# Optimization experiments

Measured on AMD Instinct MI355X. Metric: run time of the kernel, lower is better.

The kernel has to match this reference:

```python
import jax, jax.numpy as jnp
import numpy as np

B, S, HID = 2, 2048, 4096
H, KV, D = 32, 8, 128          # heads, kv heads, head_dim
G = H // KV                    # num_key_value_groups
THETA = 10000.0
SCALE = 1.0 / np.sqrt(D)
NEG_INF = -1e9


def rotate_half(x):
    x1, x2 = x[..., : D // 2], x[..., D // 2 :]
    return jnp.concatenate([-x2, x1], axis=-1)


def rope_tables(seq_len):
    inv_freq = 1.0 / (THETA ** (jnp.arange(0, D, 2, dtype=jnp.float32) / D))
    t = jnp.arange(seq_len, dtype=jnp.float32)
    freqs = jnp.outer(t, inv_freq)              # [S, D/2]
    emb = jnp.concatenate([freqs, freqs], -1)   # [S, D]
    return jnp.cos(emb), jnp.sin(emb)


def setup_inputs() -> dict:
    key = jax.random.key(0)
    ks = jax.random.split(key, 5)
    w = 0.02
    x = jax.random.normal(ks[0], (B, S, HID), jnp.float32)
    Wq = jax.random.normal(ks[1], (HID, H * D), jnp.float32) * w
    Wk = jax.random.normal(ks[2], (HID, KV * D), jnp.float32) * w
    Wv = jax.random.normal(ks[3], (HID, KV * D), jnp.float32) * w
    Wo = jax.random.normal(ks[4], (H * D, HID), jnp.float32) * w
    position_ids = jnp.broadcast_to(jnp.arange(S, dtype=jnp.int32), (B, S))
    causal = jnp.where(
        jnp.arange(S)[:, None] >= jnp.arange(S)[None, :], 0.0, NEG_INF
    ).astype(jnp.float32)
    attention_mask = jnp.broadcast_to(causal, (B, 1, S, S))
    return {
        "by_pass_hidden_states": x,
        "attention_mask": attention_mask,
        "position_ids": position_ids,
        "Wq": Wq,
        "Wk": Wk,
        "Wv": Wv,
        "Wo": Wo,
    }


def reference(by_pass_hidden_states, attention_mask, position_ids, Wq, Wk, Wv, Wo):
    x = by_pass_hidden_states
    # QKV projections (weights stored [in, out])
    q = (x @ Wq).reshape(B, S, H, D).transpose(0, 2, 1, 3)    # [B,H,S,D]
    k = (x @ Wk).reshape(B, S, KV, D).transpose(0, 2, 1, 3)   # [B,KV,S,D]
    v = (x @ Wv).reshape(B, S, KV, D).transpose(0, 2, 1, 3)   # [B,KV,S,D]
    # RoPE
    cos_t, sin_t = rope_tables(S)
    cos = cos_t[position_ids][:, None]   # [B,1,S,D]
    sin = sin_t[position_ids][:, None]
    q = q * cos + rotate_half(q) * sin
    k = k * cos + rotate_half(k) * sin
    # GQA attention without materializing repeated K/V: group query heads
    qg = q.reshape(B, KV, G, S, D)
    scores = jnp.einsum("bkgsd,bktd->bkgst", qg, k) * SCALE   # [B,KV,G,S,S]
    scores = scores.reshape(B, H, S, S) + attention_mask
    probs = jax.nn.softmax(scores.astype(jnp.float32), axis=-1).astype(x.dtype)
    ctx = jnp.einsum("bkgst,bktd->bkgsd", probs.reshape(B, KV, G, S, S), v)
    ctx = ctx.reshape(B, H, S, D).transpose(0, 2, 1, 3).reshape(B, S, H * D)
    return ctx @ Wo
```

## Files before the change

### kernel.cpp

```cpp
#include <hip/hip_runtime.h>
#include <cstdint>
#include <cstddef>

#define B_   2
#define S_   2048
#define HID_ 4096
#define H_   32
#define KV_  8
#define D_   128
#define M_   (B_*S_)
#define QSTR 6144

typedef __attribute__((ext_vector_type(8))) short bf16x8;
typedef __attribute__((ext_vector_type(4))) float f32x4;
typedef __attribute__((ext_vector_type(16))) float f32x16;
typedef __attribute__((ext_vector_type(4))) unsigned int u32x4;
typedef unsigned short u16;
typedef unsigned int   u32;

#define KSC (0.08838834764831845f * 1.4426950408889634f)

__device__ __forceinline__ float bf2f(u16 v){ u32 u = ((u32)v) << 16; return __builtin_bit_cast(float, u); }
__device__ __forceinline__ u16 f2bf(float f){
  u32 u = __builtin_bit_cast(u32, f);
  u32 r = u + 0x7fffu + ((u >> 16) & 1u);
  return (u16)(r >> 16);
}

__device__ __forceinline__ void gload_lds16(const void* g, void* lds){
  __builtin_amdgcn_global_load_lds(
      (const __attribute__((address_space(1))) void*)g,
      (__attribute__((address_space(3))) void*)lds, 16, 0, 0);
}

__global__ void cast_f32_bf16(const float* __restrict__ in, u16* __restrict__ out, int n){
  int i = (blockIdx.x * blockDim.x + threadIdx.x) * 4;
  if (i >= n) return;
  float4 v = *(const float4*)(in + i);
  ushort4 o;
  o.x = f2bf(v.x); o.y = f2bf(v.y); o.z = f2bf(v.z); o.w = f2bf(v.w);
  *(ushort4*)(out + i) = o;
}

__global__ __launch_bounds__(256) void tcast(const float* __restrict__ W, u16* __restrict__ WT,
                                             int Kd, int Nd){
  __shared__ __align__(16) u16 t[64][65];
  int k0 = blockIdx.x * 64, n0 = blockIdx.y * 64;
  int lx = threadIdx.x & 15, ly = threadIdx.x >> 4;
  #pragma unroll
  for (int rr = 0; rr < 4; ++rr){
    int r = rr * 16 + ly;
    float4 v = *(const float4*)(W + (size_t)(k0 + r) * Nd + n0 + lx * 4);
    t[lx*4+0][r] = f2bf(v.x);
    t[lx*4+1][r] = f2bf(v.y);
    t[lx*4+2][r] = f2bf(v.z);
    t[lx*4+3][r] = f2bf(v.w);
  }
  __syncthreads();
  #pragma unroll
  for (int rr = 0; rr < 4; ++rr){
    int r = rr * 16 + ly;
    ushort4 o;
    o.x = t[r][lx*4+0]; o.y = t[r][lx*4+1]; o.z = t[r][lx*4+2]; o.w = t[r][lx*4+3];
    *(ushort4*)(WT + (size_t)(n0 + r) * Kd + k0 + lx * 4) = o;
  }
}

__global__ __launch_bounds__(256) void vtrans(const u16* __restrict__ QKV, u16* __restrict__ Vt){
  __shared__ __align__(16) u16 t[64][65];
  int stile = blockIdx.x;
  int b = blockIdx.y >> 4, vt = blockIdx.y & 15;
  int s0 = stile * 64, c0 = vt * 64;
  int lx = threadIdx.x & 15, ly = threadIdx.x >> 4;
  #pragma unroll
  for (int rr = 0; rr < 4; ++rr){
    int r = rr * 16 + ly;
    ushort4 v = *(const ushort4*)(QKV + (size_t)(b*S_ + s0 + r) * QSTR + 5120 + c0 + lx*4);
    t[lx*4+0][r]=v.x; t[lx*4+1][r]=v.y; t[lx*4+2][r]=v.z; t[lx*4+3][r]=v.w;
  }
  __syncthreads();
  #pragma unroll
  for (int rr = 0; rr < 4; ++rr){
    int r = rr * 16 + ly;
    ushort4 o;
    o.x=t[r][lx*4+0]; o.y=t[r][lx*4+1]; o.z=t[r][lx*4+2]; o.w=t[r][lx*4+3];
    *(ushort4*)(Vt + (size_t)(b*1024 + c0 + r) * S_ + s0 + lx*4) = o;
  }
}

__global__ void rope_k(u16* __restrict__ X, const int* __restrict__ pos, int hshift, int stride){
  int idx = blockIdx.x * 256 + threadIdx.x;
  int i = idx & 63;
  int h = (idx >> 6) & ((1 << hshift) - 1);
  int t = idx >> (6 + hshift);
  u16* p0 = X + (size_t)t * stride + h * D_ + i;
  float x1 = bf2f(p0[0]), x2 = bf2f(p0[64]);
  float fpos = (float)pos[t];
  float invf = exp2f(-(float)(2 * i) * (13.287712379549449f / 128.0f));
  float f = fpos * invf;
  float sv = __sinf(f), cv = __cosf(f);
  p0[0]  = f2bf(x1 * cv - x2 * sv);
  p0[64] = f2bf(x2 * cv + x1 * sv);
}

#define BAR() __builtin_amdgcn_s_barrier()

#define STG_A(PB, HALF, KT) do{ \
  gload_lds16(Ag + off0 + (size_t)(HALF)*1048576 + (size_t)(KT)*128, \
              (char*)smem + (PB)*32768 + (HALF)*16384 + w*1024); \
  gload_lds16(Ag + off0 + 524288 + (size_t)(HALF)*1048576 + (size_t)(KT)*128, \
              (char*)smem + (PB)*32768 + (HALF)*16384 + 8192 + w*1024); }while(0)
#define STG_B(PB, HALF, KT) do{ \
  gload_lds16(Bg + off0 + (size_t)(HALF)*1048576 + (size_t)(KT)*128, \
              (char*)smem + 65536 + (PB)*32768 + (HALF)*16384 + w*1024); \
  gload_lds16(Bg + off0 + 524288 + (size_t)(HALF)*1048576 + (size_t)(KT)*128, \
              (char*)smem + 65536 + (PB)*32768 + (HALF)*16384 + 8192 + w*1024); }while(0)

#define RD_A(DST, PP, HALF) do{ \
  _Pragma("unroll") for (int ks = 0; ks < 2; ++ks) \
  _Pragma("unroll") for (int m = 0; m < 4; ++m) \
    DST[ks][m] = *(const bf16x8*)&smem[(PP)*16384 + (HALF)*8192 + aRowBase + m*1024 + csw[ks]]; }while(0)
#define RD_B(DST, PP, HALF) do{ \
  _Pragma("unroll") for (int ks = 0; ks < 2; ++ks) \
  _Pragma("unroll") for (int n = 0; n < 2; ++n) \
    DST[ks][n] = *(const bf16x8*)&smem[32768 + (PP)*16384 + (HALF)*8192 + bRowBase + n*1024 + csw[ks]]; }while(0)

template<int MO, int NO>
__device__ __forceinline__ void mfma_quad(f32x4 (&acc)[8][4],
                                          const bf16x8 (&af)[2][4], const bf16x8 (&bf)[2][2]){
  __builtin_amdgcn_s_setprio(1);
  #pragma unroll
  for (int ks = 0; ks < 2; ++ks)
    #pragma unroll
    for (int m = 0; m < 4; ++m)
      #pragma unroll
      for (int n = 0; n < 2; ++n)
        acc[MO+m][NO+n] = __builtin_amdgcn_mfma_f32_16x16x32_bf16(af[ks][m], bf[ks][n], acc[MO+m][NO+n], 0, 0, 0);
  __builtin_amdgcn_s_setprio(0);
}

template<bool OUTF32>
__global__ __launch_bounds__(512, 2) void gemm256(const u16* __restrict__ A, const u16* __restrict__ Bt,
                                                  void* __restrict__ C, int Nn, int mt){
  __shared__ __align__(16) u16 smem[65536];
  const int tid = threadIdx.x;
  const int l = tid & 63, w = tid >> 6;
  const int lr = l & 15, lk = l >> 4;
  const int wr = w >> 2, wc = w & 3;

  const int nwg = gridDim.x;
  const int sbid = ((int)blockIdx.x & 7) * (nwg >> 3) + ((int)blockIdx.x >> 3);
  const int bx = sbid % mt, by = sbid / mt;
  const size_t arow0 = (size_t)bx * 256;
  const size_t brow0 = (size_t)by * 256;
  const char* Ag = (const char*)(A + arow0 * 4096);
  const char* Bg = (const char*)(Bt + brow0 * 4096);

  const size_t off0 = (size_t)(w * 8 + (l >> 3)) * 8192 + (size_t)(((l & 7) ^ (l >> 3)) << 4);

  const int aRowBase = (wr*64 + lr) * 64;
  const int bRowBase = (wc*32 + lr) * 64;
  int csw[2];
  csw[0] = ((lk     ) ^ (lr & 7)) << 3;
  csw[1] = ((lk + 4) ^ (lr & 7)) << 3;

  f32x4 acc[8][4];
  #pragma unroll
  for (int i = 0; i < 8; ++i)
    #pragma unroll
    for (int j = 0; j < 4; ++j){ acc[i][j][0]=0.f; acc[i][j][1]=0.f; acc[i][j][2]=0.f; acc[i][j][3]=0.f; }

  STG_A(0, 0, 0); STG_B(0, 0, 0); STG_A(0, 1, 0); STG_B(0, 1, 0);
  STG_A(1, 0, 1); STG_B(1, 0, 1); STG_A(1, 1, 1); STG_B(1, 1, 1);
  asm volatile("s_waitcnt vmcnt(8)" ::: "memory");
  BAR();
  bf16x8 a0c[2][4], b0c[2][2], a1f[2][4], b1f[2][2];
  RD_A(a0c, 0, 0); RD_B(b0c, 0, 0);

  for (int t = 0; t < 64; ++t){
    const int P = t & 1;
    RD_A(a1f, P, 1);
    BAR();
    mfma_quad<0,0>(acc, a0c, b0c);
    BAR();
    if (t < 62){ STG_A(P, 0, t+2); STG_B(P, 0, t+2); }
    RD_B(b1f, P, 1);
    BAR();
    mfma_quad<4,0>(acc, a1f, b0c);
    BAR();
    if (t < 62){
      STG_A(P, 1, t+2);
      asm volatile("s_waitcnt vmcnt(6)" ::: "memory");
    } else if (t == 62){
      asm volatile("s_waitcnt vmcnt(0)" ::: "memory");
    }
    BAR();
    mfma_quad<4,2>(acc, a1f, b1f);
    BAR();
    if (t < 62){ STG_B(P, 1, t+2); }
    BAR();
    mfma_quad<0,2>(acc, a0c, b1f);
    if (t < 63){ RD_A(a0c, P^1, 0); RD_B(b0c, P^1, 0); }
    BAR();
  }

  #pragma unroll
  for (int mh = 0; mh < 2; ++mh)
    #pragma unroll
    for (int m = 0; m < 4; ++m)
      #pragma unroll
      for (int nh = 0; nh < 2; ++nh)
        #pragma unroll
        for (int n = 0; n < 2; ++n)
          #pragma unroll
          for (int j = 0; j < 4; ++j){
            size_t gr = arow0 + mh*128 + wr*64 + m*16 + lk*4 + j;
            size_t gc = brow0 + nh*128 + wc*32 + n*16 + lr;
            float v = acc[mh*4+m][nh*2+n][j];
            if (OUTF32) ((float*)C)[gr * Nn + gc] = v;
            else        ((u16*)C)[gr * Nn + gc] = f2bf(v);
          }
}

#define STG_B3(PB, KT) do{ \
  _Pragma("unroll") for (int r2 = 0; r2 < 3; ++r2) \
    gload_lds16(Bg + bsrc3[r2] + (size_t)(KT)*128, \
                (char*)smem + 65536 + (PB)*24576 + r2*8192 + w*1024); }while(0)

#define RD_B0(DST, PP) do{ \
  _Pragma("unroll") for (int ks = 0; ks < 2; ++ks) \
  _Pragma("unroll") for (int n = 0; n < 2; ++n) \
    DST[ks][n] = *(const bf16x8*)&smem[32768 + (PP)*12288 + bRowBase + n*1024 + csw[ks]]; }while(0)
#define RD_B1(DST, PP) do{ \
  _Pragma("unroll") for (int ks = 0; ks < 2; ++ks) \
    DST[ks] = *(const bf16x8*)&smem[32768 + (PP)*12288 + bRowBase + 2048 + csw[ks]]; }while(0)

__device__ __forceinline__ void mfma_pair16(f32x4 (&acc)[8][3], int MO,
                                            const bf16x8 (&af)[2][4], const bf16x8 (&bf)[2][2]){
  __builtin_amdgcn_s_setprio(1);
  #pragma unroll
  for (int ks = 0; ks < 2; ++ks)
    #pragma unroll
    for (int m = 0; m < 4; ++m)
      #pragma unroll
      for (int n = 0; n < 2; ++n)
        acc[MO+m][n] = __builtin_amdgcn_mfma_f32_16x16x32_bf16(af[ks][m], bf[ks][n], acc[MO+m][n], 0, 0, 0);
  __builtin_amdgcn_s_setprio(0);
}
__device__ __forceinline__ void mfma_pair8(f32x4 (&acc)[8][3], int MO,
                                           const bf16x8 (&af)[2][4], const bf16x8 (&bf)[2]){
  __builtin_amdgcn_s_setprio(1);
  #pragma unroll
  for (int ks = 0; ks < 2; ++ks)
    #pragma unroll
    for (int m = 0; m < 4; ++m)
      acc[MO+m][2] = __builtin_amdgcn_mfma_f32_16x16x32_bf16(af[ks][m], bf[ks], acc[MO+m][2], 0, 0, 0);
  __builtin_amdgcn_s_setprio(0);
}

__global__ __launch_bounds__(512, 2) void gemm192(const u16* __restrict__ A, const u16* __restrict__ Bt,
                                                  u16* __restrict__ C, int Nn, int mt){
  __shared__ __align__(16) u16 smem[57344];
  const int tid = threadIdx.x;
  const int l = tid & 63, w = tid >> 6;
  const int lr = l & 15, lk = l >> 4;
  const int wr = w >> 2, wc = w & 3;

  const int nwg = gridDim.x;
  const int sbid = ((int)blockIdx.x & 7) * (nwg >> 3) + ((int)blockIdx.x >> 3);
  const int bx = sbid % mt, by = sbid / mt;
  const size_t arow0 = (size_t)bx * 256;
  const size_t bcol0 = (size_t)by * 192;
  const char* Ag = (const char*)(A + arow0 * 4096);
  const char* Bg = (const char*)(Bt + bcol0 * 4096);

  const size_t off0 = (size_t)(w * 8 + (l >> 3)) * 8192 + (size_t)(((l & 7) ^ (l >> 3)) << 4);
  size_t bsrc3[3];
  #pragma unroll
  for (int r2 = 0; r2 < 3; ++r2){
    int idx = r2 * 512 + tid;
    int row = idx >> 3, ch = idx & 7;
    bsrc3[r2] = (size_t)row * 8192 + (size_t)((ch ^ (row & 7)) << 4);
  }

  const int aRowBase = (wr*64 + lr) * 64;
  const int bRowBase = (wc*48 + lr) * 64;
  int csw[2];
  csw[0] = ((lk     ) ^ (lr & 7)) << 3;
  csw[1] = ((lk + 4) ^ (lr & 7)) << 3;

  f32x4 acc[8][3];
  #pragma unroll
  for (int i = 0; i < 8; ++i)
    #pragma unroll
    for (int j = 0; j < 3; ++j){ acc[i][j][0]=0.f; acc[i][j][1]=0.f; acc[i][j][2]=0.f; acc[i][j][3]=0.f; }

  STG_A(0, 0, 0); STG_A(0, 1, 0); STG_B3(0, 0);
  STG_A(1, 0, 1); STG_A(1, 1, 1); STG_B3(1, 1);
  asm volatile("s_waitcnt vmcnt(7)" ::: "memory");
  BAR();
  bf16x8 a0c[2][4], a1f[2][4], b0c[2][2], b1f[2];
  RD_A(a0c, 0, 0); RD_B0(b0c, 0);

  for (int t = 0; t < 64; ++t){
    const int P = t & 1;
    RD_A(a1f, P, 1);
    BAR();
    mfma_pair16(acc, 0, a0c, b0c);
    BAR();
    if (t < 62){ STG_A(P, 0, t+2); }
    RD_B1(b1f, P);
    BAR();
    mfma_pair16(acc, 4, a1f, b0c);
    BAR();
    if (t < 62){
      STG_A(P, 1, t+2);
      asm volatile("s_waitcnt vmcnt(4)" ::: "memory");
    } else if (t == 62){
      asm volatile("s_waitcnt vmcnt(0)" ::: "memory");
    }
    BAR();
    mfma_pair8(acc, 4, a1f, b1f);
    BAR();
    if (t < 62){ STG_B3(P, t+2); }
    BAR();
    mfma_pair8(acc, 0, a0c, b1f);
    if (t < 63){ RD_A(a0c, P^1, 0); RD_B0(b0c, P^1); }
    BAR();
  }

  #pragma unroll
  for (int mh = 0; mh < 2; ++mh)
    #pragma unroll
    for (int m = 0; m < 4; ++m)
      #pragma unroll
      for (int f = 0; f < 3; ++f)
        #pragma unroll
        for (int j = 0; j < 4; ++j){
          size_t gr = arow0 + mh*128 + wr*64 + m*16 + lk*4 + j;
          size_t gc = bcol0 + wc*48 + f*16 + lr;
          C[gr * Nn + gc] = f2bf(acc[mh*4+m][f][j]);
        }
}

__global__ __launch_bounds__(512, 2) void attn_k(const u16* __restrict__ QKV,
                                                 const u16* __restrict__ Vtg,
                                                 u16* __restrict__ ctx){
  __shared__ __align__(16) u16 smem[32768];
  const int tid = threadIdx.x;
  const int l = tid & 63, w = tid >> 6;
  const int lane31 = l & 31, hi = l >> 5;
  const int hb = blockIdx.x;
  const int b = hb >> 5, h = hb & 31, kvh = h >> 2;
  const int qb = 7 - blockIdx.y;
  const int q0w = qb * 256 + w * 32;
  const int qg = q0w + lane31;

  const u16* Qp = QKV + (size_t)b * S_ * QSTR + (size_t)h * D_;
  const char* Kp = (const char*)(QKV + (size_t)b * S_ * QSTR + 4096 + (size_t)kvh * D_);
  const char* Vp = (const char*)(Vtg + ((size_t)b * 1024 + kvh * 128) * S_);

  bf16x8 qf[8];
  #pragma unroll
  for (int dt = 0; dt < 8; ++dt)
    qf[dt] = *(const bf16x8*)(Qp + (size_t)qg * QSTR + dt * 16 + hi * 8);

  const int krow0 = (2*w)*4 + (l >> 4), krow1 = krow0 + 4;
  const size_t koff0 = (size_t)krow0 * (QSTR*2) + (((l & 15) << 4) ^ ((krow0 & 7) << 4));
  const size_t koff1 = (size_t)krow1 * (QSTR*2) + (((l & 15) << 4) ^ ((krow1 & 7) << 4));
  const int vrow0 = (2*w)*8 + (l >> 3), vrow1 = vrow0 + 8;
  const size_t voff0 = (size_t)vrow0 * (S_*2) + (((l & 7) << 4) ^ ((vrow0 & 7) << 4));
  const size_t voff1 = (size_t)vrow1 * (S_*2) + (((l & 7) << 4) ^ ((vrow1 & 7) << 4));

  f32x16 acc[4];
  #pragma unroll
  for (int dt = 0; dt < 4; ++dt)
    #pragma unroll
    for (int i = 0; i < 16; ++i) acc[dt][i] = 0.f;
  float mrow = -3e38f, lsum = 0.f;

  const int nt = qb * 4 + 4;

  auto STAGE = [&](int t, int bufn){
    char* Kb = (char*)smem + bufn * 16384;
    char* Vb = (char*)smem + 32768 + bufn * 16384;
    size_t kb = (size_t)t * 64 * (QSTR*2);
    size_t vb = (size_t)t * 128;
    gload_lds16(Kp + kb + koff0, Kb + (2*w)*1024);
    gload_lds16(Kp + kb + koff1, Kb + (2*w+1)*1024);
    gload_lds16(Vp + vb + voff0, Vb + (2*w)*1024);
    gload_lds16(Vp + vb + voff1, Vb + (2*w+1)*1024);
  };

  STAGE(0, 0);
  __syncthreads();
  int buf = 0;
  for (int t = 0; t < nt; ++t){
    if (t + 1 < nt) STAGE(t + 1, buf ^ 1);
    const int kbase = t * 64;
    if (kbase <= q0w + 31){
      const char* Kb = (const char*)smem + buf * 16384;
      const char* Vb = (const char*)smem + 32768 + buf * 16384;
      const int swz = (lane31 & 7) << 4;

      f32x16 s0, s1;
      #pragma unroll
      for (int i = 0; i < 16; ++i){ s0[i] = 0.f; s1[i] = 0.f; }
      #pragma unroll
      for (int dt = 0; dt < 8; ++dt){
        bf16x8 kf = *(const bf16x8*)(Kb + lane31*256 + ((dt*32 + hi*16) ^ swz));
        s0 = __builtin_amdgcn_mfma_f32_32x32x16_bf16(kf, qf[dt], s0, 0, 0, 0);
      }
      #pragma unroll
      for (int dt = 0; dt < 8; ++dt){
        bf16x8 kf = *(const bf16x8*)(Kb + (32 + lane31)*256 + ((dt*32 + hi*16) ^ swz));
        s1 = __builtin_amdgcn_mfma_f32_32x32x16_bf16(kf, qf[dt], s1, 0, 0, 0);
      }

      if (kbase + 63 > q0w){
        int thr = qg - kbase;
        #pragma unroll
        for (int r = 0; r < 16; ++r){
          int kc = (r & 3) + 8*(r >> 2) + 4*hi;
          s0[r] = (kc > thr)      ? -1e30f : s0[r];
          s1[r] = (kc + 32 > thr) ? -1e30f : s1[r];
        }
      }

      float tmax = s0[0];
      #pragma unroll
      for (int r = 1; r < 16; ++r) tmax = fmaxf(tmax, s0[r]);
      #pragma unroll
      for (int r = 0; r < 16; ++r) tmax = fmaxf(tmax, s1[r]);
      tmax = fmaxf(tmax, __shfl_xor(tmax, 32));
      float mn = fmaxf(mrow, tmax);
      float rf = exp2f((mrow - mn) * KSC);
      mrow = mn;
      float ps = 0.f;
      #pragma unroll
      for (int r = 0; r < 16; ++r){
        float a = exp2f((s0[r] - mn) * KSC);
        float c = exp2f((s1[r] - mn) * KSC);
        s0[r] = a; s1[r] = c; ps += a + c;
      }
      ps += __shfl_xor(ps, 32);
      lsum = lsum * rf + ps;
      #pragma unroll
      for (int dt = 0; dt < 4; ++dt)
        #pragma unroll
        for (int i = 0; i < 16; ++i) acc[dt][i] *= rf;

      u32 pw[16];
      #pragma unroll
      for (int g = 0; g < 4; ++g){
        pw[2*g]     = (u32)f2bf(s0[4*g])   | ((u32)f2bf(s0[4*g+1]) << 16);
        pw[2*g+1]   = (u32)f2bf(s0[4*g+2]) | ((u32)f2bf(s0[4*g+3]) << 16);
        pw[8+2*g]   = (u32)f2bf(s1[4*g])   | ((u32)f2bf(s1[4*g+1]) << 16);
        pw[8+2*g+1] = (u32)f2bf(s1[4*g+2]) | ((u32)f2bf(s1[4*g+3]) << 16);
      }

      #pragma unroll
      for (int kt = 0; kt < 4; ++kt){
        u32 W0 = pw[kt*4+0], W1 = pw[kt*4+1], W2 = pw[kt*4+2], W3 = pw[kt*4+3];
        u32 x0 = hi ? W0 : W2;
        u32 x1 = hi ? W1 : W3;
        u32 y0 = __shfl_xor(x0, 32);
        u32 y1 = __shfl_xor(x1, 32);
        u32 w0 = hi ? y0 : W0;
        u32 w1 = hi ? y1 : W1;
        u32 w2 = hi ? W2 : y0;
        u32 w3 = hi ? W3 : y1;
        u32x4 pk; pk[0]=w0; pk[1]=w1; pk[2]=w2; pk[3]=w3;
        bf16x8 pa = __builtin_bit_cast(bf16x8, pk);
        #pragma unroll
        for (int dt = 0; dt < 4; ++dt){
          bf16x8 vf = *(const bf16x8*)(Vb + (dt*32 + lane31)*128 + ((kt*32 + hi*16) ^ swz));
          acc[dt] = __builtin_amdgcn_mfma_f32_32x32x16_bf16(vf, pa, acc[dt], 0, 0, 0);
        }
      }
    }
    __syncthreads();
    buf ^= 1;
  }

  __syncthreads();
  u16* Ot = smem + w * 4096;
  float inv = 1.f / lsum;
  #pragma unroll
  for (int dt = 0; dt < 4; ++dt)
    #pragma unroll
    for (int r = 0; r < 16; ++r){
      int d = dt*32 + (r & 3) + 8*(r >> 2) + 4*hi;
      Ot[lane31*128 + (d ^ ((lane31 & 15) << 2))] = f2bf(acc[dt][r] * inv);
    }
  u16* outp = ctx + ((size_t)(b * S_ + q0w)) * HID_ + h * D_;
  #pragma unroll
  for (int it = 0; it < 16; ++it){
    int id = it * 64 + l;
    int q = id >> 5;
    int c4 = (id & 31) * 4;
    ushort4 vv = *(const ushort4*)(Ot + q*128 + (c4 ^ ((q & 15) << 2)));
    *(ushort4*)(outp + (size_t)q * HID_ + c4) = vv;
  }
}

extern "C" void kernel_launch(void* const* d_in, const int* in_sizes, int n_in,
                              void* d_out, int out_size, void* d_ws, size_t ws_size,
                              hipStream_t stream) {
  const float* x  = (const float*)d_in[0];
  const int*   pos = (const int*)d_in[2];
  const float* Wq = (const float*)d_in[3];
  const float* Wk = (const float*)d_in[4];
  const float* Wv = (const float*)d_in[5];
  const float* Wo = (const float*)d_in[6];

  char* ws = (char*)d_ws;
  u16* xb   = (u16*)(ws);
  u16* WT   = (u16*)(ws + ((size_t)32 << 20));
  u16* WoT  = (u16*)(ws + ((size_t)80 << 20));
  u16* QKVb = (u16*)(ws + ((size_t)112 << 20));
  u16* Vtg  = (u16*)(ws + ((size_t)32 << 20));

  cast_f32_bf16<<<16384, 256, 0, stream>>>(x, xb, HID_ * M_);
  tcast<<<dim3(64, 64), 256, 0, stream>>>(Wq, WT, 4096, 4096);
  tcast<<<dim3(64, 16), 256, 0, stream>>>(Wk, WT + (size_t)4096 * 4096, 4096, 1024);
  tcast<<<dim3(64, 16), 256, 0, stream>>>(Wv, WT + (size_t)5120 * 4096, 4096, 1024);
  tcast<<<dim3(64, 64), 256, 0, stream>>>(Wo, WoT, 4096, 4096);
  gemm192<<<512, 512, 0, stream>>>(xb, WT, QKVb, 6144, 16);
  rope_k<<<32768, 256, 0, stream>>>(QKVb,        pos, 5, QSTR);
  rope_k<<<8192,  256, 0, stream>>>(QKVb + 4096, pos, 3, QSTR);
  vtrans<<<dim3(32, 32), 256, 0, stream>>>(QKVb, Vtg);
  attn_k<<<dim3(64, 8), 512, 0, stream>>>(QKVb, Vtg, xb);
  gemm256<true><<<256, 512, 0, stream>>>(xb, WoT, d_out, 4096, 16);
}
```

Before: 517.2 us.

## Fuse Q RoPE into attention, lazy softmax rescale, unroll GEMM loops by two

```diff
diff --git a/kernel.cpp b/kernel.cpp
--- a/kernel.cpp
+++ b/kernel.cpp
@@ -139,6 +139,32 @@
   __builtin_amdgcn_s_setprio(0);
 }
 
+#define G256_TILE(P, TT) do{                                             \
+  RD_A(a1f, P, 1);                                                       \
+  BAR();                                                                 \
+  mfma_quad<0,0>(acc, a0c, b0c);                                         \
+  BAR();                                                                 \
+  if ((TT) < 62){ STG_A(P, 0, (TT)+2); STG_B(P, 0, (TT)+2); }            \
+  RD_B(b1f, P, 1);                                                       \
+  BAR();                                                                 \
+  mfma_quad<4,0>(acc, a1f, b0c);                                         \
+  BAR();                                                                 \
+  if ((TT) < 62){                                                        \
+    STG_A(P, 1, (TT)+2);                                                 \
+    asm volatile("s_waitcnt vmcnt(6)" ::: "memory");                     \
+  } else if ((TT) == 62){                                                \
+    asm volatile("s_waitcnt vmcnt(0)" ::: "memory");                     \
+  }                                                                      \
+  BAR();                                                                 \
+  mfma_quad<4,2>(acc, a1f, b1f);                                         \
+  BAR();                                                                 \
+  if ((TT) < 62){ STG_B(P, 1, (TT)+2); }                                 \
+  BAR();                                                                 \
+  mfma_quad<0,2>(acc, a0c, b1f);                                         \
+  if ((TT) < 63){ RD_A(a0c, (P)^1, 0); RD_B(b0c, (P)^1, 0); }            \
+  BAR();                                                                 \
+}while(0)
+
 template<bool OUTF32>
 __global__ __launch_bounds__(512, 2) void gemm256(const u16* __restrict__ A, const u16* __restrict__ Bt,
                                                   void* __restrict__ C, int Nn, int mt){
@@ -177,31 +203,9 @@
   bf16x8 a0c[2][4], b0c[2][2], a1f[2][4], b1f[2][2];
   RD_A(a0c, 0, 0); RD_B(b0c, 0, 0);
 
-  for (int t = 0; t < 64; ++t){
-    const int P = t & 1;
-    RD_A(a1f, P, 1);
-    BAR();
-    mfma_quad<0,0>(acc, a0c, b0c);
-    BAR();
-    if (t < 62){ STG_A(P, 0, t+2); STG_B(P, 0, t+2); }
-    RD_B(b1f, P, 1);
-    BAR();
-    mfma_quad<4,0>(acc, a1f, b0c);
-    BAR();
-    if (t < 62){
-      STG_A(P, 1, t+2);
-      asm volatile("s_waitcnt vmcnt(6)" ::: "memory");
-    } else if (t == 62){
-      asm volatile("s_waitcnt vmcnt(0)" ::: "memory");
-    }
-    BAR();
-    mfma_quad<4,2>(acc, a1f, b1f);
-    BAR();
-    if (t < 62){ STG_B(P, 1, t+2); }
-    BAR();
-    mfma_quad<0,2>(acc, a0c, b1f);
-    if (t < 63){ RD_A(a0c, P^1, 0); RD_B(b0c, P^1, 0); }
-    BAR();
+  for (int t = 0; t < 64; t += 2){
+    G256_TILE(0, t);
+    G256_TILE(1, t+1);
   }
 
   #pragma unroll
@@ -258,6 +262,32 @@
   __builtin_amdgcn_s_setprio(0);
 }
 
+#define G192_TILE(P, TT) do{                                             \
+  RD_A(a1f, P, 1);                                                       \
+  BAR();                                                                 \
+  mfma_pair16(acc, 0, a0c, b0c);                                         \
+  BAR();                                                                 \
+  if ((TT) < 62){ STG_A(P, 0, (TT)+2); }                                 \
+  RD_B1(b1f, P);                                                         \
+  BAR();                                                                 \
+  mfma_pair16(acc, 4, a1f, b0c);                                         \
+  BAR();                                                                 \
+  if ((TT) < 62){                                                        \
+    STG_A(P, 1, (TT)+2);                                                 \
+    asm volatile("s_waitcnt vmcnt(4)" ::: "memory");                     \
+  } else if ((TT) == 62){                                                \
+    asm volatile("s_waitcnt vmcnt(0)" ::: "memory");                     \
+  }                                                                      \
+  BAR();                                                                 \
+  mfma_pair8(acc, 4, a1f, b1f);                                          \
+  BAR();                                                                 \
+  if ((TT) < 62){ STG_B3(P, (TT)+2); }                                   \
+  BAR();                                                                 \
+  mfma_pair8(acc, 0, a0c, b1f);                                          \
+  if ((TT) < 63){ RD_A(a0c, (P)^1, 0); RD_B0(b0c, (P)^1); }              \
+  BAR();                                                                 \
+}while(0)
+
 __global__ __launch_bounds__(512, 2) void gemm192(const u16* __restrict__ A, const u16* __restrict__ Bt,
                                                   u16* __restrict__ C, int Nn, int mt){
   __shared__ __align__(16) u16 smem[57344];
@@ -302,31 +332,9 @@
   bf16x8 a0c[2][4], a1f[2][4], b0c[2][2], b1f[2];
   RD_A(a0c, 0, 0); RD_B0(b0c, 0);
 
-  for (int t = 0; t < 64; ++t){
-    const int P = t & 1;
-    RD_A(a1f, P, 1);
-    BAR();
-    mfma_pair16(acc, 0, a0c, b0c);
-    BAR();
-    if (t < 62){ STG_A(P, 0, t+2); }
-    RD_B1(b1f, P);
-    BAR();
-    mfma_pair16(acc, 4, a1f, b0c);
-    BAR();
-    if (t < 62){
-      STG_A(P, 1, t+2);
-      asm volatile("s_waitcnt vmcnt(4)" ::: "memory");
-    } else if (t == 62){
-      asm volatile("s_waitcnt vmcnt(0)" ::: "memory");
-    }
-    BAR();
-    mfma_pair8(acc, 4, a1f, b1f);
-    BAR();
-    if (t < 62){ STG_B3(P, t+2); }
-    BAR();
-    mfma_pair8(acc, 0, a0c, b1f);
-    if (t < 63){ RD_A(a0c, P^1, 0); RD_B0(b0c, P^1); }
-    BAR();
+  for (int t = 0; t < 64; t += 2){
+    G192_TILE(0, t);
+    G192_TILE(1, t+1);
   }
 
   #pragma unroll
@@ -345,6 +353,7 @@
 
 __global__ __launch_bounds__(512, 2) void attn_k(const u16* __restrict__ QKV,
                                                  const u16* __restrict__ Vtg,
+                                                 const int* __restrict__ pos,
                                                  u16* __restrict__ ctx){
   __shared__ __align__(16) u16 smem[32768];
   const int tid = threadIdx.x;
@@ -352,7 +361,8 @@
   const int lane31 = l & 31, hi = l >> 5;
   const int hb = blockIdx.x;
   const int b = hb >> 5, h = hb & 31, kvh = h >> 2;
-  const int qb = 7 - blockIdx.y;
+  const int y = blockIdx.y;
+  const int qb = (y < 4) ? (7 - y) : (y - 4);
   const int q0w = qb * 256 + w * 32;
   const int qg = q0w + lane31;
 
@@ -364,6 +374,25 @@
   #pragma unroll
   for (int dt = 0; dt < 8; ++dt)
     qf[dt] = *(const bf16x8*)(Qp + (size_t)qg * QSTR + dt * 16 + hi * 8);
+
+  {
+    float fp = (float)pos[b * S_ + qg];
+    #pragma unroll
+    for (int dt = 0; dt < 4; ++dt){
+      bf16x8 lo = qf[dt], hi8 = qf[dt + 4], nlo, nhi;
+      #pragma unroll
+      for (int j = 0; j < 8; ++j){
+        int d = dt * 16 + hi * 8 + j;
+        float invf = exp2f(-(float)(2 * d) * (13.287712379549449f / 128.0f));
+        float f = fp * invf;
+        float sv = __sinf(f), cv = __cosf(f);
+        float x1 = bf2f((u16)lo[j]), x2 = bf2f((u16)hi8[j]);
+        nlo[j] = (short)f2bf(x1 * cv - x2 * sv);
+        nhi[j] = (short)f2bf(x2 * cv + x1 * sv);
+      }
+      qf[dt] = nlo; qf[dt + 4] = nhi;
+    }
+  }
 
   const int krow0 = (2*w)*4 + (l >> 4), krow1 = krow0 + 4;
   const size_t koff0 = (size_t)krow0 * (QSTR*2) + (((l & 15) << 4) ^ ((krow0 & 7) << 4));
@@ -433,22 +462,25 @@
       #pragma unroll
       for (int r = 0; r < 16; ++r) tmax = fmaxf(tmax, s1[r]);
       tmax = fmaxf(tmax, __shfl_xor(tmax, 32));
-      float mn = fmaxf(mrow, tmax);
-      float rf = exp2f((mrow - mn) * KSC);
-      mrow = mn;
+      if (!__all(tmax - mrow <= 62.7f)){
+        float mn = fmaxf(mrow, tmax);
+        float rf = exp2f((mrow - mn) * KSC);
+        mrow = mn;
+        lsum *= rf;
+        #pragma unroll
+        for (int dt = 0; dt < 4; ++dt)
+          #pragma unroll
+          for (int i = 0; i < 16; ++i) acc[dt][i] *= rf;
+      }
       float ps = 0.f;
       #pragma unroll
       for (int r = 0; r < 16; ++r){
-        float a = exp2f((s0[r] - mn) * KSC);
-        float c = exp2f((s1[r] - mn) * KSC);
+        float a = exp2f((s0[r] - mrow) * KSC);
+        float c = exp2f((s1[r] - mrow) * KSC);
         s0[r] = a; s1[r] = c; ps += a + c;
       }
       ps += __shfl_xor(ps, 32);
-      lsum = lsum * rf + ps;
-      #pragma unroll
-      for (int dt = 0; dt < 4; ++dt)
-        #pragma unroll
-        for (int i = 0; i < 16; ++i) acc[dt][i] *= rf;
+      lsum += ps;
 
       u32 pw[16];
       #pragma unroll
@@ -527,9 +559,8 @@
   tcast<<<dim3(64, 16), 256, 0, stream>>>(Wv, WT + (size_t)5120 * 4096, 4096, 1024);
   tcast<<<dim3(64, 64), 256, 0, stream>>>(Wo, WoT, 4096, 4096);
   gemm192<<<512, 512, 0, stream>>>(xb, WT, QKVb, 6144, 16);
-  rope_k<<<32768, 256, 0, stream>>>(QKVb,        pos, 5, QSTR);
-  rope_k<<<8192,  256, 0, stream>>>(QKVb + 4096, pos, 3, QSTR);
+  rope_k<<<8192, 256, 0, stream>>>(QKVb + 4096, pos, 3, QSTR);
   vtrans<<<dim3(32, 32), 256, 0, stream>>>(QKVb, Vtg);
-  attn_k<<<dim3(64, 8), 512, 0, stream>>>(QKVb, Vtg, xb);
+  attn_k<<<dim3(64, 8), 512, 0, stream>>>(QKVb, Vtg, pos, xb);
   gemm256<true><<<256, 512, 0, stream>>>(xb, WoT, d_out, 4096, 16);
 }
```

Result: slower. 722.9 us (+39.8%).
